# Performance work log

Hardware: AMD Instinct MI355X
Metric: run time of the kernel (lower is better)

## Reference

```python
import jax, jax.numpy as jnp
import numpy as np

D_MODEL = 192
D_STATE = 16
D_CONV = 3
D_INNER = 384  # expand * d_model
DT_RANK = 12   # ceil(d_model / 16)
BATCH = 8
SEQLEN = 4096


def setup_inputs() -> dict:
    key = jax.random.key(0)
    ks = jax.random.split(key, 8)
    s = 0.02
    dt_init_std = DT_RANK ** (-0.5)
    return {
        "hidden_states": jax.random.normal(ks[0], (BATCH, SEQLEN, D_MODEL), jnp.float32),
        "in_proj_w": jax.random.normal(ks[1], (2 * D_INNER, D_MODEL), jnp.float32) * s,
        "conv_w": jax.random.normal(ks[2], (D_INNER, 1, D_CONV), jnp.float32) * 0.1,
        "conv_b": jnp.zeros((D_INNER,), jnp.float32),
        "x_proj_w": jax.random.normal(ks[3], (DT_RANK + 2 * D_STATE, D_INNER), jnp.float32) * s,
        "dt_proj_w": jax.random.uniform(ks[4], (D_INNER, DT_RANK), jnp.float32, -dt_init_std, dt_init_std),
        "dt_proj_b": jax.random.uniform(ks[5], (D_INNER,), jnp.float32, -5.0, -2.0),
        "A_log": jnp.tile(jnp.log(jnp.arange(1, D_STATE + 1, dtype=jnp.float32))[None, :], (D_INNER, 1)),
        "D_skip": jnp.ones((D_INNER,), jnp.float32),
        "out_proj_w": jax.random.normal(ks[6], (D_MODEL, D_INNER), jnp.float32) * s,
    }


def reference(hidden_states, in_proj_w, conv_w, conv_b, x_proj_w,
              dt_proj_w, dt_proj_b, A_log, D_skip, out_proj_w):
    # in_proj: [B,L,d_model] -> [B,L,2*d_inner]
    xz = jnp.einsum('bld,ed->ble', hidden_states, in_proj_w)
    x, z = jnp.split(xz, 2, axis=-1)
    # depthwise conv1d over sequence, 'same' padding for kernel 3
    xc = jnp.transpose(x, (0, 2, 1))  # [B, d_inner, L]
    pad = (D_CONV - 1) // 2
    xc = jax.lax.conv_general_dilated(
        xc, conv_w, window_strides=(1,), padding=[(pad, pad)],
        feature_group_count=D_INNER, dimension_numbers=('NCH', 'OIH', 'NCH'))
    xc = xc + conv_b[None, :, None]
    x = jax.nn.silu(jnp.transpose(xc, (0, 2, 1)))  # [B, L, d_inner]
    # x_proj -> dt, B, C
    x_dbl = jnp.einsum('bld,ed->ble', x, x_proj_w)
    dt = x_dbl[..., :DT_RANK]
    Bm = x_dbl[..., DT_RANK:DT_RANK + D_STATE]
    Cm = x_dbl[..., DT_RANK + D_STATE:]
    dt = jnp.einsum('blr,dr->bld', dt, dt_proj_w) + dt_proj_b  # Linear adds bias
    dt = jax.nn.softplus(dt + dt_proj_b)  # original adds bias AGAIN inside scan (faithful)
    A = -jnp.exp(A_log)  # [d_inner, d_state]
    # selective scan over time (sequential recurrence -> lax.scan)
    xs = (jnp.swapaxes(dt, 0, 1), jnp.swapaxes(Bm, 0, 1),
          jnp.swapaxes(Cm, 0, 1), jnp.swapaxes(x, 0, 1))
    h0 = jnp.zeros((hidden_states.shape[0], D_INNER, D_STATE), x.dtype)

    def step(h, ts):
        dt_i, B_i, C_i, u_i = ts  # [B,d], [B,n], [B,n], [B,d]
        A_disc = jnp.exp(dt_i[:, :, None] * A[None])        # [B,d,n]
        h = A_disc * h + (dt_i * u_i)[:, :, None] * B_i[:, None, :]
        y = jnp.einsum('bdn,bn->bd', h, C_i) + D_skip * u_i
        return h, y

    _, ys = jax.lax.scan(step, h0, xs)  # ys: [L, B, d_inner]
    y = jnp.swapaxes(ys, 0, 1)
    y = y * jax.nn.silu(z)
    return jnp.einsum('bld,ed->ble', y, out_proj_w)
```

## Files before the change

### kernel.cpp

```cpp
#include <hip/hip_runtime.h>
#include <cmath>

#define BATCH 8
#define SEQLEN 4096
#define DMODEL 192
#define DINNER 384
#define DSTATE 16
#define DTRANK 12
#define XSTR 64
#define MTOT (BATCH*SEQLEN)
#define CH 32
#define NC (SEQLEN/CH)

typedef __bf16 bf16x8 __attribute__((ext_vector_type(8)));
typedef float f32x4 __attribute__((ext_vector_type(4)));
typedef unsigned short us8 __attribute__((ext_vector_type(8)));

__device__ __forceinline__ float fast_rcp(float x) { return __builtin_amdgcn_rcpf(x); }
__device__ __forceinline__ float silu_f(float x) { return x * fast_rcp(1.f + __expf(-x)); }
__device__ __forceinline__ unsigned short f2bf(float f) {
  unsigned u = __float_as_uint(f);
  return (unsigned short)((u + 0x7FFF + ((u >> 16) & 1)) >> 16);
}
__device__ __forceinline__ float bf2f(unsigned short b) {
  return __uint_as_float(((unsigned)b) << 16);
}

#define POW16(a, e1)                                                        \
  a[0] = (e1); a[1] = (e1) * (e1); a[2] = a[1] * (e1); a[3] = a[1] * a[1];  \
  a[4] = a[3] * (e1); a[5] = a[3] * a[1]; a[6] = a[3] * a[2];               \
  a[7] = a[3] * a[3]; a[8] = a[7] * (e1); a[9] = a[7] * a[1];               \
  a[10] = a[7] * a[2]; a[11] = a[7] * a[3]; a[12] = a[7] * a[4];            \
  a[13] = a[7] * a[5]; a[14] = a[7] * a[6]; a[15] = a[7] * a[7];

#define SOFTPLUS_E1(s, dtv, e1)                                             \
  { const float w_ = __expf(-fabsf(s));                                     \
    const float t_ = 1.f + w_;                                              \
    const float rq_ = fast_rcp(t_);                                         \
    dtv = fmaxf(s, 0.f) + __logf(t_);                                       \
    e1 = (s > 0.f) ? w_ * rq_ : rq_; }

__global__ __launch_bounds__(256) void prep_k(const float* __restrict__ in_w,
                                              const float* __restrict__ xw,
                                              const float* __restrict__ ow,
                                              unsigned short* __restrict__ wb,
                                              unsigned short* __restrict__ wxb,
                                              unsigned short* __restrict__ owb) {
  const int i = blockIdx.x * 256 + threadIdx.x;
  if (i < 768 * DMODEL) wb[i] = f2bf(in_w[i]);
  if (i < XSTR * DINNER) wxb[i] = (i < 44 * DINNER) ? f2bf(xw[i]) : (unsigned short)0;
  if (i < DMODEL * DINNER) owb[i] = f2bf(ow[i]);
}

__global__ __launch_bounds__(256) void gemm_in(const float* __restrict__ hs,
                                               const unsigned short* __restrict__ wb,
                                               unsigned short* __restrict__ xb,
                                               unsigned short* __restrict__ zb) {
  __shared__ unsigned short Als[128 * 40];
  __shared__ unsigned short Bls[128 * 40];
  const int tid = threadIdx.x;
  const int bid = blockIdx.y * 6 + blockIdx.x;
  const int lid = (bid & 7) * 192 + (bid >> 3);
  const int m0 = (lid / 6) * 128, n0 = (lid % 6) * 128;
  const int w = tid >> 6, l = tid & 63;
  const int wm = (w >> 1) * 64, wn = (w & 1) * 64;
  const int lr = l & 15, lk8 = (l >> 4) * 8;
  const int ar = tid >> 1, ag = (tid & 1) * 16;
  const float* Ap = hs + (size_t)(m0 + ar) * DMODEL + ag;
  const unsigned short* Wp = wb + (size_t)(n0 + ar) * DMODEL + ag;
  f32x4 acc[4][4];
#pragma unroll
  for (int i = 0; i < 4; i++)
#pragma unroll
    for (int j = 0; j < 4; j++) acc[i][j] = (f32x4){0.f, 0.f, 0.f, 0.f};
#pragma unroll
  for (int k0 = 0; k0 < DMODEL; k0 += 32) {
    float4 f0 = *(const float4*)(Ap + k0);
    float4 f1 = *(const float4*)(Ap + k0 + 4);
    float4 f2 = *(const float4*)(Ap + k0 + 8);
    float4 f3 = *(const float4*)(Ap + k0 + 12);
    us8 b0 = *(const us8*)(Wp + k0);
    us8 b1 = *(const us8*)(Wp + k0 + 8);
    us8 a0, a1;
    a0[0] = f2bf(f0.x); a0[1] = f2bf(f0.y); a0[2] = f2bf(f0.z); a0[3] = f2bf(f0.w);
    a0[4] = f2bf(f1.x); a0[5] = f2bf(f1.y); a0[6] = f2bf(f1.z); a0[7] = f2bf(f1.w);
    a1[0] = f2bf(f2.x); a1[1] = f2bf(f2.y); a1[2] = f2bf(f2.z); a1[3] = f2bf(f2.w);
    a1[4] = f2bf(f3.x); a1[5] = f2bf(f3.y); a1[6] = f2bf(f3.z); a1[7] = f2bf(f3.w);
    __syncthreads();
    *(us8*)(&Als[ar * 40 + ag]) = a0;
    *(us8*)(&Als[ar * 40 + ag + 8]) = a1;
    *(us8*)(&Bls[ar * 40 + ag]) = b0;
    *(us8*)(&Bls[ar * 40 + ag + 8]) = b1;
    __syncthreads();
    bf16x8 bfr[4];
#pragma unroll
    for (int fn = 0; fn < 4; fn++)
      bfr[fn] = *(const bf16x8*)(&Bls[(wn + fn * 16 + lr) * 40 + lk8]);
#pragma unroll
    for (int fm = 0; fm < 4; fm++) {
      bf16x8 af = *(const bf16x8*)(&Als[(wm + fm * 16 + lr) * 40 + lk8]);
#pragma unroll
      for (int fn = 0; fn < 4; fn++)
        acc[fm][fn] = __builtin_amdgcn_mfma_f32_16x16x32_bf16(af, bfr[fn], acc[fm][fn], 0, 0, 0);
    }
  }
  const int r0 = (l >> 4) * 4;
  unsigned short* dst = (n0 < DINNER) ? xb : zb;
  const int cb0 = (n0 < DINNER) ? n0 : (n0 - DINNER);
#pragma unroll
  for (int fm = 0; fm < 4; fm++) {
    const size_t rowb = (size_t)(m0 + wm + fm * 16 + r0);
#pragma unroll
    for (int fn = 0; fn < 4; fn++) {
      const int col = cb0 + wn + fn * 16 + lr;
#pragma unroll
      for (int r = 0; r < 4; r++)
        dst[(rowb + r) * DINNER + col] = f2bf(acc[fm][fn][r]);
    }
  }
}

__global__ __launch_bounds__(256) void conv_silu_k(const unsigned short* __restrict__ xb,
                                                   const float* __restrict__ cw,
                                                   const float* __restrict__ cb,
                                                   unsigned short* __restrict__ u16) {
  __shared__ float cws[DINNER * 4];
  const int tid = threadIdx.x;
  for (int i = tid; i < DINNER * 4; i += 256)
    cws[i] = (i < DINNER * 3) ? cw[i] : cb[i - DINNER * 3];
  __syncthreads();
  const int idx = blockIdx.x * 256 + tid;
  const int d = (idx % 48) * 8;
  const int m = idx / 48;
  const int l = m % SEQLEN;
  const us8 c0 = *(const us8*)(xb + (size_t)m * DINNER + d);
  const bool hm = (l > 0), hp = (l < SEQLEN - 1);
  us8 cm = c0, cp = c0;
  if (hm) cm = *(const us8*)(xb + (size_t)(m - 1) * DINNER + d);
  if (hp) cp = *(const us8*)(xb + (size_t)(m + 1) * DINNER + d);
  us8 o;
#pragma unroll
  for (int j = 0; j < 8; j++) {
    const int dj = d + j;
    float s = cws[DINNER * 3 + dj] + cws[dj * 3 + 1] * bf2f(c0[j]);
    if (hm) s += cws[dj * 3 + 0] * bf2f(cm[j]);
    if (hp) s += cws[dj * 3 + 2] * bf2f(cp[j]);
    o[j] = f2bf(silu_f(s));
  }
  *(us8*)(u16 + (size_t)m * DINNER + d) = o;
}

__global__ __launch_bounds__(256) void xproj_mfma(const unsigned short* __restrict__ u16,
                                                  const unsigned short* __restrict__ wxb,
                                                  float* __restrict__ xdbl) {
  __shared__ unsigned short Als[64 * 40];
  __shared__ unsigned short Bls[64 * 40];
  const int tid = threadIdx.x;
  const int m0 = blockIdx.x * 64;
  const int w = tid >> 6, l = tid & 63;
  const int wm = (w >> 1) * 32, wn = (w & 1) * 32;
  const int lr = l & 15, lk8 = (l >> 4) * 8;
  const int ar = tid >> 2, ag = (tid & 3) * 8;
  const unsigned short* Ap = u16 + (size_t)(m0 + ar) * DINNER + ag;
  const unsigned short* Wp = wxb + (size_t)ar * DINNER + ag;
  f32x4 acc[2][2];
#pragma unroll
  for (int i = 0; i < 2; i++)
#pragma unroll
    for (int j = 0; j < 2; j++) acc[i][j] = (f32x4){0.f, 0.f, 0.f, 0.f};
#pragma unroll
  for (int k0 = 0; k0 < DINNER; k0 += 32) {
    us8 a0 = *(const us8*)(Ap + k0);
    us8 b0 = *(const us8*)(Wp + k0);
    __syncthreads();
    *(us8*)(&Als[ar * 40 + ag]) = a0;
    *(us8*)(&Bls[ar * 40 + ag]) = b0;
    __syncthreads();
    bf16x8 bf0 = *(const bf16x8*)(&Bls[(wn + lr) * 40 + lk8]);
    bf16x8 bf1 = *(const bf16x8*)(&Bls[(wn + 16 + lr) * 40 + lk8]);
#pragma unroll
    for (int fm = 0; fm < 2; fm++) {
      bf16x8 af = *(const bf16x8*)(&Als[(wm + fm * 16 + lr) * 40 + lk8]);
      acc[fm][0] = __builtin_amdgcn_mfma_f32_16x16x32_bf16(af, bf0, acc[fm][0], 0, 0, 0);
      acc[fm][1] = __builtin_amdgcn_mfma_f32_16x16x32_bf16(af, bf1, acc[fm][1], 0, 0, 0);
    }
  }
  const int r0 = (l >> 4) * 4;
#pragma unroll
  for (int fm = 0; fm < 2; fm++) {
    const size_t rowb = (size_t)(m0 + wm + fm * 16 + r0);
#pragma unroll
    for (int fn = 0; fn < 2; fn++) {
      const int col = wn + fn * 16 + lr;
#pragma unroll
      for (int r = 0; r < 4; r++)
        xdbl[(rowb + r) * XSTR + col] = acc[fm][fn][r];
    }
  }
}

__global__ __launch_bounds__(384, 6) void scan_part1(const unsigned short* __restrict__ u16,
                                                     const float* __restrict__ xdbl,
                                                     const float* __restrict__ A_log,
                                                     const float* __restrict__ dtw,
                                                     const float* __restrict__ dtb,
                                                     float* __restrict__ Pbuf,
                                                     float* __restrict__ Sbuf) {
  __shared__ float XL[CH * 32];
  const int d = threadIdx.x;
  const int c = blockIdx.x, b = blockIdx.y;
  const size_t mbase = (size_t)b * SEQLEN + (size_t)c * CH;
  if (d < CH * 7) {
    const int r = d / 7, q = d % 7;
    float4 v = *(const float4*)(xdbl + (mbase + r) * XSTR + q * 4);
    *(float4*)(&XL[r * 32 + q * 4]) = v;
  }
  float wr[DTRANK];
#pragma unroll
  for (int q = 0; q < 3; q++)
    *(float4*)(wr + q * 4) = *(const float4*)(dtw + d * DTRANK + q * 4);
  const float b2 = 2.f * dtb[d];
  bool fastp = true;
#pragma unroll
  for (int n = 0; n < DSTATE; n++)
    fastp = fastp && (fabsf(A_log[d * DSTATE + n] - __logf((float)(n + 1))) < 1e-5f);
  float h[DSTATE];
#pragma unroll
  for (int n = 0; n < DSTATE; n++) h[n] = 0.f;
  __syncthreads();
  float uv = bf2f(u16[mbase * DINNER + d]);
  float P[DSTATE];
  if (fastp) {
    float Pprod = 1.f;
    for (int l = 0; l < CH; l++) {
      const int lp = (l + 1 < CH) ? (l + 1) : l;
      const float un = bf2f(u16[(mbase + lp) * DINNER + d]);
      const float* Lr = &XL[l * 32];
      float s = b2;
#pragma unroll
      for (int r = 0; r < DTRANK; r++) s = fmaf(Lr[r], wr[r], s);
      float dtv, e1;
      SOFTPLUS_E1(s, dtv, e1)
      const float du = dtv * uv;
      Pprod *= e1;
      float a[DSTATE];
      POW16(a, e1)
#pragma unroll
      for (int n = 0; n < DSTATE; n++)
        h[n] = fmaf(a[n], h[n], du * Lr[12 + n]);
      uv = un;
    }
    POW16(P, Pprod)
  } else {
    float Av[DSTATE];
#pragma unroll
    for (int n = 0; n < DSTATE; n++) Av[n] = -__expf(A_log[d * DSTATE + n]);
    float dtsum = 0.f;
    for (int l = 0; l < CH; l++) {
      const int lp = (l + 1 < CH) ? (l + 1) : l;
      const float un = bf2f(u16[(mbase + lp) * DINNER + d]);
      const float* Lr = &XL[l * 32];
      float s = b2;
#pragma unroll
      for (int r = 0; r < DTRANK; r++) s = fmaf(Lr[r], wr[r], s);
      float dtv, e1;
      SOFTPLUS_E1(s, dtv, e1)
      (void)e1;
      const float du = dtv * uv;
      dtsum += dtv;
#pragma unroll
      for (int n = 0; n < DSTATE; n++)
        h[n] = fmaf(__expf(dtv * Av[n]), h[n], du * Lr[12 + n]);
      uv = un;
    }
#pragma unroll
    for (int n = 0; n < DSTATE; n++) P[n] = __expf(dtsum * Av[n]);
  }
  float* Pp = Pbuf + ((size_t)(b * NC + c) * DINNER + d) * DSTATE;
  float* Sp = Sbuf + ((size_t)(b * NC + c) * DINNER + d) * DSTATE;
#pragma unroll
  for (int q = 0; q < 4; q++) {
    float4 pv, sv;
    pv.x = P[q * 4 + 0]; pv.y = P[q * 4 + 1]; pv.z = P[q * 4 + 2]; pv.w = P[q * 4 + 3];
    sv.x = h[q * 4 + 0]; sv.y = h[q * 4 + 1]; sv.z = h[q * 4 + 2]; sv.w = h[q * 4 + 3];
    *(float4*)(Pp + q * 4) = pv;
    *(float4*)(Sp + q * 4) = sv;
  }
}

__global__ __launch_bounds__(256) void scan_part2(float* __restrict__ Pbuf,
                                                  const float* __restrict__ Sbuf) {
  const int i = blockIdx.x * 256 + threadIdx.x;
  const int b = i / (DINNER * DSTATE);
  const int r = i % (DINNER * DSTATE);
  const size_t cs = DINNER * DSTATE;
  const size_t base = (size_t)b * NC * cs + r;
  float h = 0.f;
  for (int c0 = 0; c0 < NC; c0 += 8) {
    float pp[8], ss[8];
#pragma unroll
    for (int j = 0; j < 8; j++) {
      pp[j] = Pbuf[base + (size_t)(c0 + j) * cs];
      ss[j] = Sbuf[base + (size_t)(c0 + j) * cs];
    }
#pragma unroll
    for (int j = 0; j < 8; j++) {
      Pbuf[base + (size_t)(c0 + j) * cs] = h;
      h = fmaf(pp[j], h, ss[j]);
    }
  }
}

__global__ __launch_bounds__(384, 6) void scan_part3(const unsigned short* __restrict__ u16,
                                                     const float* __restrict__ xdbl,
                                                     const float* __restrict__ A_log,
                                                     const float* __restrict__ dtw,
                                                     const float* __restrict__ dtb,
                                                     const float* __restrict__ Dsk,
                                                     const unsigned short* __restrict__ zb,
                                                     const float* __restrict__ H0,
                                                     unsigned short* __restrict__ yb) {
  __shared__ float XL[CH * 48];
  const int d = threadIdx.x;
  const int c = blockIdx.x, b = blockIdx.y;
  const size_t mbase = (size_t)b * SEQLEN + (size_t)c * CH;
  if (d < CH * 11) {
    const int r = d / 11, q = d % 11;
    float4 v = *(const float4*)(xdbl + (mbase + r) * XSTR + q * 4);
    *(float4*)(&XL[r * 48 + q * 4]) = v;
  }
  float wr[DTRANK];
#pragma unroll
  for (int q = 0; q < 3; q++)
    *(float4*)(wr + q * 4) = *(const float4*)(dtw + d * DTRANK + q * 4);
  const float b2 = 2.f * dtb[d];
  bool fastp = true;
#pragma unroll
  for (int n = 0; n < DSTATE; n++)
    fastp = fastp && (fabsf(A_log[d * DSTATE + n] - __logf((float)(n + 1))) < 1e-5f);
  const float Dv = Dsk[d];
  float h[DSTATE];
  {
    const float* Hp = H0 + ((size_t)(b * NC + c) * DINNER + d) * DSTATE;
#pragma unroll
    for (int q = 0; q < 4; q++) {
      float4 v = *(const float4*)(Hp + q * 4);
      h[q * 4 + 0] = v.x; h[q * 4 + 1] = v.y; h[q * 4 + 2] = v.z; h[q * 4 + 3] = v.w;
    }
  }
  __syncthreads();
  float uv = bf2f(u16[mbase * DINNER + d]);
  float zv = bf2f(zb[mbase * DINNER + d]);
  if (fastp) {
    for (int l = 0; l < CH; l++) {
      const int lp = (l + 1 < CH) ? (l + 1) : l;
      const float un = bf2f(u16[(mbase + lp) * DINNER + d]);
      const float zn = bf2f(zb[(mbase + lp) * DINNER + d]);
      const float* Lr = &XL[l * 48];
      float s = b2;
#pragma unroll
      for (int r = 0; r < DTRANK; r++) s = fmaf(Lr[r], wr[r], s);
      float dtv, e1;
      SOFTPLUS_E1(s, dtv, e1)
      const float du = dtv * uv;
      float a[DSTATE];
      POW16(a, e1)
      float y0 = Dv * uv, y1 = 0.f, y2 = 0.f, y3 = 0.f;
#pragma unroll
      for (int n = 0; n < DSTATE; n += 4) {
        h[n + 0] = fmaf(a[n + 0], h[n + 0], du * Lr[12 + n + 0]);
        h[n + 1] = fmaf(a[n + 1], h[n + 1], du * Lr[12 + n + 1]);
        h[n + 2] = fmaf(a[n + 2], h[n + 2], du * Lr[12 + n + 2]);
        h[n + 3] = fmaf(a[n + 3], h[n + 3], du * Lr[12 + n + 3]);
        y0 = fmaf(h[n + 0], Lr[28 + n + 0], y0);
        y1 = fmaf(h[n + 1], Lr[28 + n + 1], y1);
        y2 = fmaf(h[n + 2], Lr[28 + n + 2], y2);
        y3 = fmaf(h[n + 3], Lr[28 + n + 3], y3);
      }
      const float yacc = (y0 + y1) + (y2 + y3);
      yb[(mbase + l) * DINNER + d] = f2bf(yacc * silu_f(zv));
      uv = un; zv = zn;
    }
  } else {
    float Av[DSTATE];
#pragma unroll
    for (int n = 0; n < DSTATE; n++) Av[n] = -__expf(A_log[d * DSTATE + n]);
    for (int l = 0; l < CH; l++) {
      const int lp = (l + 1 < CH) ? (l + 1) : l;
      const float un = bf2f(u16[(mbase + lp) * DINNER + d]);
      const float zn = bf2f(zb[(mbase + lp) * DINNER + d]);
      const float* Lr = &XL[l * 48];
      float s = b2;
#pragma unroll
      for (int r = 0; r < DTRANK; r++) s = fmaf(Lr[r], wr[r], s);
      float dtv, e1;
      SOFTPLUS_E1(s, dtv, e1)
      (void)e1;
      const float du = dtv * uv;
      float yacc = Dv * uv;
#pragma unroll
      for (int n = 0; n < DSTATE; n++) {
        h[n] = fmaf(__expf(dtv * Av[n]), h[n], du * Lr[12 + n]);
        yacc = fmaf(h[n], Lr[28 + n], yacc);
      }
      yb[(mbase + l) * DINNER + d] = f2bf(yacc * silu_f(zv));
      uv = un; zv = zn;
    }
  }
}

__global__ __launch_bounds__(256) void gemm_out(const unsigned short* __restrict__ yb,
                                                const unsigned short* __restrict__ owb,
                                                float* __restrict__ out) {
  __shared__ unsigned short Als[128 * 40];
  __shared__ unsigned short Bls[64 * 40];
  const int tid = threadIdx.x;
  const int bid = blockIdx.y * 3 + blockIdx.x;
  const int lid = (bid & 7) * 96 + (bid >> 3);
  const int m0 = (lid / 3) * 128, n0 = (lid % 3) * 64;
  const int w = tid >> 6, l = tid & 63;
  const int wm = (w >> 1) * 64, wn = (w & 1) * 32;
  const int lr = l & 15, lk8 = (l >> 4) * 8;
  const int ar = tid >> 1, ag = (tid & 1) * 16;
  const int br = tid >> 2, bg = (tid & 3) * 8;
  const unsigned short* Ap = yb + (size_t)(m0 + ar) * DINNER + ag;
  const unsigned short* Wp = owb + (size_t)(n0 + br) * DINNER + bg;
  f32x4 acc[4][2];
#pragma unroll
  for (int i = 0; i < 4; i++)
#pragma unroll
    for (int j = 0; j < 2; j++) acc[i][j] = (f32x4){0.f, 0.f, 0.f, 0.f};
#pragma unroll
  for (int k0 = 0; k0 < DINNER; k0 += 32) {
    us8 a0 = *(const us8*)(Ap + k0);
    us8 a1 = *(const us8*)(Ap + k0 + 8);
    us8 bv = *(const us8*)(Wp + k0);
    __syncthreads();
    *(us8*)(&Als[ar * 40 + ag]) = a0;
    *(us8*)(&Als[ar * 40 + ag + 8]) = a1;
    *(us8*)(&Bls[br * 40 + bg]) = bv;
    __syncthreads();
    bf16x8 b0 = *(const bf16x8*)(&Bls[(wn + lr) * 40 + lk8]);
    bf16x8 b1 = *(const bf16x8*)(&Bls[(wn + 16 + lr) * 40 + lk8]);
#pragma unroll
    for (int fm = 0; fm < 4; fm++) {
      bf16x8 af = *(const bf16x8*)(&Als[(wm + fm * 16 + lr) * 40 + lk8]);
      acc[fm][0] = __builtin_amdgcn_mfma_f32_16x16x32_bf16(af, b0, acc[fm][0], 0, 0, 0);
      acc[fm][1] = __builtin_amdgcn_mfma_f32_16x16x32_bf16(af, b1, acc[fm][1], 0, 0, 0);
    }
  }
  const int r0 = (l >> 4) * 4;
#pragma unroll
  for (int fm = 0; fm < 4; fm++) {
    const size_t rowb = (size_t)(m0 + wm + fm * 16 + r0);
#pragma unroll
    for (int fn = 0; fn < 2; fn++) {
      const int col = n0 + wn + fn * 16 + lr;
#pragma unroll
      for (int r = 0; r < 4; r++)
        out[(rowb + r) * DMODEL + col] = acc[fm][fn][r];
    }
  }
}

extern "C" void kernel_launch(void* const* d_in, const int* in_sizes, int n_in,
                              void* d_out, int out_size, void* d_ws, size_t ws_size,
                              hipStream_t stream) {
  const float* hs   = (const float*)d_in[0];
  const float* in_w = (const float*)d_in[1];
  const float* cw   = (const float*)d_in[2];
  const float* cb   = (const float*)d_in[3];
  const float* xw   = (const float*)d_in[4];
  const float* dtw  = (const float*)d_in[5];
  const float* dtb  = (const float*)d_in[6];
  const float* alog = (const float*)d_in[7];
  const float* dsk  = (const float*)d_in[8];
  const float* ow   = (const float*)d_in[9];
  float* out = (float*)d_out;

  char* ws = (char*)d_ws;
  unsigned short* xb  = (unsigned short*)(ws);
  unsigned short* u16 = (unsigned short*)(ws + 25165824);
  float* xdbl = (float*)(ws + 50331648);
  float* Pbuf = (float*)(ws + 58720256);
  float* Sbuf = (float*)(ws + 83886080);
  unsigned short* zb  = (unsigned short*)(ws + 109051904);
  unsigned short* wb  = (unsigned short*)(ws + 134217728);
  unsigned short* wxb = (unsigned short*)(ws + 134512640);
  unsigned short* owb = (unsigned short*)(ws + 134561792);
  unsigned short* yb  = xb;

  prep_k<<<576, 256, 0, stream>>>(in_w, xw, ow, wb, wxb, owb);
  gemm_in<<<dim3(6, 256), 256, 0, stream>>>(hs, wb, xb, zb);
  conv_silu_k<<<(MTOT * 48) / 256, 256, 0, stream>>>(xb, cw, cb, u16);
  xproj_mfma<<<MTOT / 64, 256, 0, stream>>>(u16, wxb, xdbl);
  scan_part1<<<dim3(NC, BATCH), 384, 0, stream>>>(u16, xdbl, alog, dtw, dtb, Pbuf, Sbuf);
  scan_part2<<<(BATCH * DINNER * DSTATE) / 256, 256, 0, stream>>>(Pbuf, Sbuf);
  scan_part3<<<dim3(NC, BATCH), 384, 0, stream>>>(u16, xdbl, alog, dtw, dtb, dsk, zb, Pbuf, yb);
  gemm_out<<<dim3(3, 256), 256, 0, stream>>>(yb, owb, out);
}
```

Before: 200.2 us.

## Fuse conv+SiLU into x_proj GEMM and batch scan timesteps in groups of eight

Merges the depthwise conv/SiLU kernel into the x_proj MFMA kernel: the conv output is computed on the fly from xb, fed to the GEMM, and also written to u16. This removes one launch and one re-read of u16. The scan kernels now precompute the softplus, decay and input terms for eight timesteps before running the recurrence, use float4 shared loads and a split dt dot product, and have their launch-bounds occupancy hint lowered from 6 to 4 to allow more registers. The fused kernel does extra neighbour-row loads per tile, and the batched scan raises register pressure.

```diff
diff --git a/kernel.cpp b/kernel.cpp
--- a/kernel.cpp
+++ b/kernel.cpp
@@ -38,7 +38,21 @@
     const float t_ = 1.f + w_;                                              \
     const float rq_ = fast_rcp(t_);                                         \
     dtv = fmaxf(s, 0.f) + __logf(t_);                                       \
-    e1 = (s > 0.f) ? w_ * rq_ : rq_; }
+    e1 = ((s) > 0.f) ? w_ * rq_ : rq_; }
+
+__device__ __forceinline__ float dot12(const float* __restrict__ Lr,
+                                       const float* __restrict__ wr, float b2) {
+  float4 x0 = *(const float4*)(Lr);
+  float4 x1 = *(const float4*)(Lr + 4);
+  float4 x2 = *(const float4*)(Lr + 8);
+  float sA = fmaf(x0.x, wr[0], b2);
+  sA = fmaf(x0.y, wr[1], sA); sA = fmaf(x0.z, wr[2], sA); sA = fmaf(x0.w, wr[3], sA);
+  float sB = x1.x * wr[4];
+  sB = fmaf(x1.y, wr[5], sB); sB = fmaf(x1.z, wr[6], sB); sB = fmaf(x1.w, wr[7], sB);
+  float sC = x2.x * wr[8];
+  sC = fmaf(x2.y, wr[9], sC); sC = fmaf(x2.z, wr[10], sC); sC = fmaf(x2.w, wr[11], sC);
+  return sA + (sB + sC);
+}
 
 __global__ __launch_bounds__(256) void prep_k(const float* __restrict__ in_w,
                                               const float* __restrict__ xw,
@@ -120,58 +134,51 @@
   }
 }
 
-__global__ __launch_bounds__(256) void conv_silu_k(const unsigned short* __restrict__ xb,
-                                                   const float* __restrict__ cw,
-                                                   const float* __restrict__ cb,
-                                                   unsigned short* __restrict__ u16) {
+__global__ __launch_bounds__(256) void xproj_conv(const unsigned short* __restrict__ xb,
+                                                  const float* __restrict__ cw,
+                                                  const float* __restrict__ cb,
+                                                  const unsigned short* __restrict__ wxb,
+                                                  float* __restrict__ xdbl,
+                                                  unsigned short* __restrict__ u16) {
+  __shared__ unsigned short Als[64 * 40];
+  __shared__ unsigned short Bls[64 * 40];
   __shared__ float cws[DINNER * 4];
   const int tid = threadIdx.x;
+  const int m0 = blockIdx.x * 64;
   for (int i = tid; i < DINNER * 4; i += 256)
     cws[i] = (i < DINNER * 3) ? cw[i] : cb[i - DINNER * 3];
-  __syncthreads();
-  const int idx = blockIdx.x * 256 + tid;
-  const int d = (idx % 48) * 8;
-  const int m = idx / 48;
-  const int l = m % SEQLEN;
-  const us8 c0 = *(const us8*)(xb + (size_t)m * DINNER + d);
-  const bool hm = (l > 0), hp = (l < SEQLEN - 1);
-  us8 cm = c0, cp = c0;
-  if (hm) cm = *(const us8*)(xb + (size_t)(m - 1) * DINNER + d);
-  if (hp) cp = *(const us8*)(xb + (size_t)(m + 1) * DINNER + d);
-  us8 o;
-#pragma unroll
-  for (int j = 0; j < 8; j++) {
-    const int dj = d + j;
-    float s = cws[DINNER * 3 + dj] + cws[dj * 3 + 1] * bf2f(c0[j]);
-    if (hm) s += cws[dj * 3 + 0] * bf2f(cm[j]);
-    if (hp) s += cws[dj * 3 + 2] * bf2f(cp[j]);
-    o[j] = f2bf(silu_f(s));
-  }
-  *(us8*)(u16 + (size_t)m * DINNER + d) = o;
-}
-
-__global__ __launch_bounds__(256) void xproj_mfma(const unsigned short* __restrict__ u16,
-                                                  const unsigned short* __restrict__ wxb,
-                                                  float* __restrict__ xdbl) {
-  __shared__ unsigned short Als[64 * 40];
-  __shared__ unsigned short Bls[64 * 40];
-  const int tid = threadIdx.x;
-  const int m0 = blockIdx.x * 64;
   const int w = tid >> 6, l = tid & 63;
   const int wm = (w >> 1) * 32, wn = (w & 1) * 32;
   const int lr = l & 15, lk8 = (l >> 4) * 8;
   const int ar = tid >> 2, ag = (tid & 3) * 8;
-  const unsigned short* Ap = u16 + (size_t)(m0 + ar) * DINNER + ag;
+  const int m = m0 + ar;
+  const int lpos = m % SEQLEN;
+  const bool hm = (lpos > 0), hp = (lpos < SEQLEN - 1);
+  const unsigned short* Ap = xb + (size_t)m * DINNER + ag;
   const unsigned short* Wp = wxb + (size_t)ar * DINNER + ag;
   f32x4 acc[2][2];
 #pragma unroll
   for (int i = 0; i < 2; i++)
 #pragma unroll
     for (int j = 0; j < 2; j++) acc[i][j] = (f32x4){0.f, 0.f, 0.f, 0.f};
+  __syncthreads();
 #pragma unroll
   for (int k0 = 0; k0 < DINNER; k0 += 32) {
-    us8 a0 = *(const us8*)(Ap + k0);
+    us8 c0 = *(const us8*)(Ap + k0);
+    us8 cm = c0, cp = c0;
+    if (hm) cm = *(const us8*)(Ap + k0 - DINNER);
+    if (hp) cp = *(const us8*)(Ap + k0 + DINNER);
     us8 b0 = *(const us8*)(Wp + k0);
+    us8 a0;
+#pragma unroll
+    for (int j = 0; j < 8; j++) {
+      const int col = ag + k0 + j;
+      float s = cws[DINNER * 3 + col] + cws[col * 3 + 1] * bf2f(c0[j]);
+      if (hm) s += cws[col * 3 + 0] * bf2f(cm[j]);
+      if (hp) s += cws[col * 3 + 2] * bf2f(cp[j]);
+      a0[j] = f2bf(silu_f(s));
+    }
+    *(us8*)(u16 + (size_t)m * DINNER + ag + k0) = a0;
     __syncthreads();
     *(us8*)(&Als[ar * 40 + ag]) = a0;
     *(us8*)(&Bls[ar * 40 + ag]) = b0;
@@ -199,7 +206,7 @@
   }
 }
 
-__global__ __launch_bounds__(384, 6) void scan_part1(const unsigned short* __restrict__ u16,
+__global__ __launch_bounds__(384, 4) void scan_part1(const unsigned short* __restrict__ u16,
                                                      const float* __restrict__ xdbl,
                                                      const float* __restrict__ A_log,
                                                      const float* __restrict__ dtw,
@@ -228,27 +235,43 @@
 #pragma unroll
   for (int n = 0; n < DSTATE; n++) h[n] = 0.f;
   __syncthreads();
-  float uv = bf2f(u16[mbase * DINNER + d]);
   float P[DSTATE];
   if (fastp) {
     float Pprod = 1.f;
-    for (int l = 0; l < CH; l++) {
-      const int lp = (l + 1 < CH) ? (l + 1) : l;
-      const float un = bf2f(u16[(mbase + lp) * DINNER + d]);
-      const float* Lr = &XL[l * 32];
-      float s = b2;
-#pragma unroll
-      for (int r = 0; r < DTRANK; r++) s = fmaf(Lr[r], wr[r], s);
-      float dtv, e1;
-      SOFTPLUS_E1(s, dtv, e1)
-      const float du = dtv * uv;
-      Pprod *= e1;
-      float a[DSTATE];
-      POW16(a, e1)
-#pragma unroll
-      for (int n = 0; n < DSTATE; n++)
-        h[n] = fmaf(a[n], h[n], du * Lr[12 + n]);
-      uv = un;
+    for (int g = 0; g < CH / 8; g++) {
+      float e18[8], du8[8];
+#pragma unroll
+      for (int j = 0; j < 8; j++) {
+        const int l = g * 8 + j;
+        const float s = dot12(&XL[l * 32], wr, b2);
+        const float uvj = bf2f(u16[(mbase + l) * DINNER + d]);
+        float dtv, e1;
+        SOFTPLUS_E1(s, dtv, e1)
+        e18[j] = e1;
+        du8[j] = dtv * uvj;
+      }
+      Pprod *= ((e18[0] * e18[1]) * (e18[2] * e18[3])) *
+               ((e18[4] * e18[5]) * (e18[6] * e18[7]));
+#pragma unroll
+      for (int j = 0; j < 8; j++) {
+        const int l = g * 8 + j;
+        const float* Lr = &XL[l * 32 + 12];
+        float4 B0 = *(const float4*)(Lr);
+        float4 B1 = *(const float4*)(Lr + 4);
+        float4 B2 = *(const float4*)(Lr + 8);
+        float4 B3 = *(const float4*)(Lr + 12);
+        float a[DSTATE];
+        POW16(a, e18[j])
+        const float du = du8[j];
+        h[0]  = fmaf(a[0],  h[0],  du * B0.x); h[1]  = fmaf(a[1],  h[1],  du * B0.y);
+        h[2]  = fmaf(a[2],  h[2],  du * B0.z); h[3]  = fmaf(a[3],  h[3],  du * B0.w);
+        h[4]  = fmaf(a[4],  h[4],  du * B1.x); h[5]  = fmaf(a[5],  h[5],  du * B1.y);
+        h[6]  = fmaf(a[6],  h[6],  du * B1.z); h[7]  = fmaf(a[7],  h[7],  du * B1.w);
+        h[8]  = fmaf(a[8],  h[8],  du * B2.x); h[9]  = fmaf(a[9],  h[9],  du * B2.y);
+        h[10] = fmaf(a[10], h[10], du * B2.z); h[11] = fmaf(a[11], h[11], du * B2.w);
+        h[12] = fmaf(a[12], h[12], du * B3.x); h[13] = fmaf(a[13], h[13], du * B3.y);
+        h[14] = fmaf(a[14], h[14], du * B3.z); h[15] = fmaf(a[15], h[15], du * B3.w);
+      }
     }
     POW16(P, Pprod)
   } else {
@@ -257,12 +280,9 @@
     for (int n = 0; n < DSTATE; n++) Av[n] = -__expf(A_log[d * DSTATE + n]);
     float dtsum = 0.f;
     for (int l = 0; l < CH; l++) {
-      const int lp = (l + 1 < CH) ? (l + 1) : l;
-      const float un = bf2f(u16[(mbase + lp) * DINNER + d]);
+      const float uv = bf2f(u16[(mbase + l) * DINNER + d]);
       const float* Lr = &XL[l * 32];
-      float s = b2;
-#pragma unroll
-      for (int r = 0; r < DTRANK; r++) s = fmaf(Lr[r], wr[r], s);
+      const float s = dot12(Lr, wr, b2);
       float dtv, e1;
       SOFTPLUS_E1(s, dtv, e1)
       (void)e1;
@@ -271,7 +291,6 @@
 #pragma unroll
       for (int n = 0; n < DSTATE; n++)
         h[n] = fmaf(__expf(dtv * Av[n]), h[n], du * Lr[12 + n]);
-      uv = un;
     }
 #pragma unroll
     for (int n = 0; n < DSTATE; n++) P[n] = __expf(dtsum * Av[n]);
@@ -311,7 +330,7 @@
   }
 }
 
-__global__ __launch_bounds__(384, 6) void scan_part3(const unsigned short* __restrict__ u16,
+__global__ __launch_bounds__(384, 4) void scan_part3(const unsigned short* __restrict__ u16,
                                                      const float* __restrict__ xdbl,
                                                      const float* __restrict__ A_log,
                                                      const float* __restrict__ dtw,
@@ -349,50 +368,67 @@
     }
   }
   __syncthreads();
-  float uv = bf2f(u16[mbase * DINNER + d]);
-  float zv = bf2f(zb[mbase * DINNER + d]);
   if (fastp) {
-    for (int l = 0; l < CH; l++) {
-      const int lp = (l + 1 < CH) ? (l + 1) : l;
-      const float un = bf2f(u16[(mbase + lp) * DINNER + d]);
-      const float zn = bf2f(zb[(mbase + lp) * DINNER + d]);
-      const float* Lr = &XL[l * 48];
-      float s = b2;
-#pragma unroll
-      for (int r = 0; r < DTRANK; r++) s = fmaf(Lr[r], wr[r], s);
-      float dtv, e1;
-      SOFTPLUS_E1(s, dtv, e1)
-      const float du = dtv * uv;
-      float a[DSTATE];
-      POW16(a, e1)
-      float y0 = Dv * uv, y1 = 0.f, y2 = 0.f, y3 = 0.f;
-#pragma unroll
-      for (int n = 0; n < DSTATE; n += 4) {
-        h[n + 0] = fmaf(a[n + 0], h[n + 0], du * Lr[12 + n + 0]);
-        h[n + 1] = fmaf(a[n + 1], h[n + 1], du * Lr[12 + n + 1]);
-        h[n + 2] = fmaf(a[n + 2], h[n + 2], du * Lr[12 + n + 2]);
-        h[n + 3] = fmaf(a[n + 3], h[n + 3], du * Lr[12 + n + 3]);
-        y0 = fmaf(h[n + 0], Lr[28 + n + 0], y0);
-        y1 = fmaf(h[n + 1], Lr[28 + n + 1], y1);
-        y2 = fmaf(h[n + 2], Lr[28 + n + 2], y2);
-        y3 = fmaf(h[n + 3], Lr[28 + n + 3], y3);
+    for (int g = 0; g < CH / 8; g++) {
+      float e18[8], du8[8], uD8[8], sz8[8];
+#pragma unroll
+      for (int j = 0; j < 8; j++) {
+        const int l = g * 8 + j;
+        const float s = dot12(&XL[l * 48], wr, b2);
+        const float uvj = bf2f(u16[(mbase + l) * DINNER + d]);
+        const float zvj = bf2f(zb[(mbase + l) * DINNER + d]);
+        float dtv, e1;
+        SOFTPLUS_E1(s, dtv, e1)
+        e18[j] = e1;
+        du8[j] = dtv * uvj;
+        uD8[j] = Dv * uvj;
+        sz8[j] = silu_f(zvj);
       }
-      const float yacc = (y0 + y1) + (y2 + y3);
-      yb[(mbase + l) * DINNER + d] = f2bf(yacc * silu_f(zv));
-      uv = un; zv = zn;
+#pragma unroll
+      for (int j = 0; j < 8; j++) {
+        const int l = g * 8 + j;
+        const float* Lr = &XL[l * 48 + 12];
+        float4 B0 = *(const float4*)(Lr);
+        float4 B1 = *(const float4*)(Lr + 4);
+        float4 B2 = *(const float4*)(Lr + 8);
+        float4 B3 = *(const float4*)(Lr + 12);
+        float4 C0 = *(const float4*)(Lr + 16);
+        float4 C1 = *(const float4*)(Lr + 20);
+        float4 C2 = *(const float4*)(Lr + 24);
+        float4 C3 = *(const float4*)(Lr + 28);
+        float a[DSTATE];
+        POW16(a, e18[j])
+        const float du = du8[j];
+        float y0 = uD8[j], y1 = 0.f, y2 = 0.f, y3 = 0.f;
+        h[0]  = fmaf(a[0],  h[0],  du * B0.x); y0 = fmaf(h[0],  C0.x, y0);
+        h[1]  = fmaf(a[1],  h[1],  du * B0.y); y1 = fmaf(h[1],  C0.y, y1);
+        h[2]  = fmaf(a[2],  h[2],  du * B0.z); y2 = fmaf(h[2],  C0.z, y2);
+        h[3]  = fmaf(a[3],  h[3],  du * B0.w); y3 = fmaf(h[3],  C0.w, y3);
+        h[4]  = fmaf(a[4],  h[4],  du * B1.x); y0 = fmaf(h[4],  C1.x, y0);
+        h[5]  = fmaf(a[5],  h[5],  du * B1.y); y1 = fmaf(h[5],  C1.y, y1);
+        h[6]  = fmaf(a[6],  h[6],  du * B1.z); y2 = fmaf(h[6],  C1.z, y2);
+        h[7]  = fmaf(a[7],  h[7],  du * B1.w); y3 = fmaf(h[7],  C1.w, y3);
+        h[8]  = fmaf(a[8],  h[8],  du * B2.x); y0 = fmaf(h[8],  C2.x, y0);
+        h[9]  = fmaf(a[9],  h[9],  du * B2.y); y1 = fmaf(h[9],  C2.y, y1);
+        h[10] = fmaf(a[10], h[10], du * B2.z); y2 = fmaf(h[10], C2.z, y2);
+        h[11] = fmaf(a[11], h[11], du * B2.w); y3 = fmaf(h[11], C2.w, y3);
+        h[12] = fmaf(a[12], h[12], du * B3.x); y0 = fmaf(h[12], C3.x, y0);
+        h[13] = fmaf(a[13], h[13], du * B3.y); y1 = fmaf(h[13], C3.y, y1);
+        h[14] = fmaf(a[14], h[14], du * B3.z); y2 = fmaf(h[14], C3.z, y2);
+        h[15] = fmaf(a[15], h[15], du * B3.w); y3 = fmaf(h[15], C3.w, y3);
+        const float yacc = (y0 + y1) + (y2 + y3);
+        yb[(mbase + l) * DINNER + d] = f2bf(yacc * sz8[j]);
+      }
     }
   } else {
     float Av[DSTATE];
 #pragma unroll
     for (int n = 0; n < DSTATE; n++) Av[n] = -__expf(A_log[d * DSTATE + n]);
     for (int l = 0; l < CH; l++) {
-      const int lp = (l + 1 < CH) ? (l + 1) : l;
-      const float un = bf2f(u16[(mbase + lp) * DINNER + d]);
-      const float zn = bf2f(zb[(mbase + lp) * DINNER + d]);
+      const float uv = bf2f(u16[(mbase + l) * DINNER + d]);
+      const float zv = bf2f(zb[(mbase + l) * DINNER + d]);
       const float* Lr = &XL[l * 48];
-      float s = b2;
-#pragma unroll
-      for (int r = 0; r < DTRANK; r++) s = fmaf(Lr[r], wr[r], s);
+      const float s = dot12(Lr, wr, b2);
       float dtv, e1;
       SOFTPLUS_E1(s, dtv, e1)
       (void)e1;
@@ -404,7 +440,6 @@
         yacc = fmaf(h[n], Lr[28 + n], yacc);
       }
       yb[(mbase + l) * DINNER + d] = f2bf(yacc * silu_f(zv));
-      uv = un; zv = zn;
     }
   }
 }
@@ -492,8 +527,7 @@
 
   prep_k<<<576, 256, 0, stream>>>(in_w, xw, ow, wb, wxb, owb);
   gemm_in<<<dim3(6, 256), 256, 0, stream>>>(hs, wb, xb, zb);
-  conv_silu_k<<<(MTOT * 48) / 256, 256, 0, stream>>>(xb, cw, cb, u16);
-  xproj_mfma<<<MTOT / 64, 256, 0, stream>>>(u16, wxb, xdbl);
+  xproj_conv<<<MTOT / 64, 256, 0, stream>>>(xb, cw, cb, wxb, xdbl, u16);
   scan_part1<<<dim3(NC, BATCH), 384, 0, stream>>>(u16, xdbl, alog, dtw, dtb, Pbuf, Sbuf);
   scan_part2<<<(BATCH * DINNER * DSTATE) / 256, 256, 0, stream>>>(Pbuf, Sbuf);
   scan_part3<<<dim3(NC, BATCH), 384, 0, stream>>>(u16, xdbl, alog, dtw, dtb, dsk, zb, Pbuf, yb);
```

Result: slower. 268.3 us (+34.0%).
